# Optimization experiments

Hardware: AMD Instinct MI355X
Metric: run time of the kernel (lower is better)

The kernel has to match this reference:

```python
import jax, jax.numpy as jnp
import numpy as np

D_MODEL = 1024
MEM_HEADS = 4
MEM_KNN = 32
KEY_DIM = 288
VALUE_DIM = 512
Q_RANK = 512
MEM_N_KEYS = 512
TOTAL_KEYS = MEM_N_KEYS * MEM_N_KEYS        # 262144
NUM_BUCKETS = int(np.log2(TOTAL_KEYS))      # 18
BUCKET_DIM = KEY_DIM // NUM_BUCKETS         # 16
BATCH, SEQ = 4, 512


def setup_inputs() -> dict:
    key = jax.random.key(0)
    ks = jax.random.split(key, 7)
    bound = 1.0 / np.sqrt(BUCKET_DIM)
    return {
        "x": jax.random.normal(ks[0], (BATCH, SEQ, D_MODEL), dtype=jnp.float32),
        "keys": jax.random.uniform(ks[1], (MEM_HEADS, NUM_BUCKETS, 2, BUCKET_DIM),
                                   minval=-bound, maxval=bound, dtype=jnp.float32),
        "qd_w": jax.random.normal(ks[2], (Q_RANK, D_MODEL), dtype=jnp.float32) * (1.0 / np.sqrt(D_MODEL)),
        "qd_b": jnp.zeros((Q_RANK,), dtype=jnp.float32),
        "qu_w": jax.random.normal(ks[3], (MEM_HEADS * KEY_DIM, Q_RANK), dtype=jnp.float32) * (1.0 / np.sqrt(Q_RANK)),
        "values": jax.random.normal(ks[4], (TOTAL_KEYS, VALUE_DIM), dtype=jnp.float32) * (VALUE_DIM ** -0.5),
        "vp_w": jax.random.normal(ks[5], (D_MODEL, VALUE_DIM), dtype=jnp.float32) * (1.0 / np.sqrt(VALUE_DIM)),
    }


def _get_indices(query, keys, knn):
    # query: [rows_tok, H, key_dim] flattened per head below. Here query comes
    # in as [N*H, key_dim] reshaped to [N, H, M, bucket_dim].
    N = query.shape[0]
    q = query.reshape(N, MEM_HEADS, NUM_BUCKETS, BUCKET_DIM)
    local = jnp.einsum("nhmd,hmcd->nhmc", q, keys)          # [N,H,M,2]
    s0, s1 = local[..., 0], local[..., 1]
    best_bits = s1 > s0                                      # [N,H,M]
    best_scores = jnp.maximum(s0, s1).sum(-1)                # [N,H]
    deltas = jnp.abs(s0 - s1)                                # [N,H,M]
    bit_weights = (1 << jnp.arange(NUM_BUCKETS, dtype=jnp.int32))
    best_codes = (best_bits.astype(jnp.int32) * bit_weights).sum(-1)  # [N,H]

    rows = N * MEM_HEADS
    deltas = deltas.reshape(rows, NUM_BUCKETS)
    best_scores = best_scores.reshape(rows, 1)
    best_codes = best_codes.reshape(rows, 1)
    knn_eff = min(knn, 1 << NUM_BUCKETS)

    penalties = jnp.zeros((rows, 1), dtype=jnp.float32)
    masks = jnp.zeros((rows, 1), dtype=jnp.int32)
    # Trellis search: unrolled Python loop over a small fixed bucket count (18);
    # candidate width grows 2,4,... then saturates at 2*knn -> static shapes.
    for t in range(NUM_BUCKETS):
        cand_pen = jnp.concatenate([penalties, penalties + deltas[:, t:t + 1]], axis=1)
        cand_msk = jnp.concatenate([masks, masks ^ bit_weights[t]], axis=1)
        step_k = min(knn_eff, cand_pen.shape[1])
        neg_pen, keep = jax.lax.top_k(-cand_pen, step_k)     # smallest penalties, sorted asc
        penalties = -neg_pen
        masks = jnp.take_along_axis(cand_msk, keep, axis=1)
    return best_scores - penalties, best_codes ^ masks        # [rows,knn], [rows,knn]


def reference(x, keys, qd_w, qd_b, qu_w, values, vp_w):
    B, S, D = x.shape
    N = B * S
    x_flat = x.reshape(N, D)
    q = (x_flat @ qd_w.T + qd_b) @ qu_w.T                    # [N, H*key_dim]
    scores, indices = _get_indices(q.reshape(N, MEM_HEADS, KEY_DIM), keys, MEM_KNN)
    scores = jax.nn.softmax(scores, axis=-1)                 # [N*H, knn]
    indices = indices.reshape(N, MEM_HEADS * MEM_KNN)
    scores = scores.reshape(N, MEM_HEADS * MEM_KNN)
    gathered = values[indices]                               # [N, H*knn, value_dim]
    y = jnp.einsum("nk,nkd->nd", scores, gathered)           # embedding_bag mode='sum'
    y = y @ vp_w.T                                           # value_proj (value_dim != d_model)
    return y.reshape(B, S, D_MODEL)
```

## Files before the change

### kernel.cpp

```cpp
#include <hip/hip_runtime.h>
#include <math.h>

#define D_MODEL 1024
#define MEM_HEADS 4
#define KNN 32
#define KEY_DIM 288
#define VALUE_DIM 512
#define Q_RANK 512
#define NUM_BUCKETS 18
#define BUCKET_DIM 16
#define NTOK 2048
#define ROWS (NTOK * MEM_HEADS)
#define QDIM (MEM_HEADS * KEY_DIM)

__global__ __launch_bounds__(256) void gemm_nt_kernel(
    const float* __restrict__ A, const float* __restrict__ B,
    const float* __restrict__ bias, float* __restrict__ C,
    int M, int N, int K)
{
    __shared__ __align__(16) float As[16][68];
    __shared__ __align__(16) float Bs[16][68];

    const int tid  = threadIdx.x;
    const int bm   = blockIdx.y * 64;
    const int bn   = blockIdx.x * 64;
    const int lrow = tid >> 2;
    const int lk   = (tid & 3) * 4;
    const int ty   = tid >> 4;
    const int tx   = tid & 15;

    const float* Aptr = A + (size_t)(bm + lrow) * K + lk;
    const float* Bptr = B + (size_t)(bn + lrow) * K + lk;

    float acc[4][4];
#pragma unroll
    for (int i = 0; i < 4; ++i)
#pragma unroll
        for (int j = 0; j < 4; ++j) acc[i][j] = 0.f;

    for (int k0 = 0; k0 < K; k0 += 16) {
        const float4 a4 = *(const float4*)(Aptr + k0);
        const float4 b4 = *(const float4*)(Bptr + k0);
        __syncthreads();
        As[lk + 0][lrow] = a4.x; As[lk + 1][lrow] = a4.y;
        As[lk + 2][lrow] = a4.z; As[lk + 3][lrow] = a4.w;
        Bs[lk + 0][lrow] = b4.x; Bs[lk + 1][lrow] = b4.y;
        Bs[lk + 2][lrow] = b4.z; Bs[lk + 3][lrow] = b4.w;
        __syncthreads();
#pragma unroll
        for (int kk = 0; kk < 16; ++kk) {
            const float4 af = *(const float4*)&As[kk][ty * 4];
            const float4 bf = *(const float4*)&Bs[kk][tx * 4];
            const float a[4] = {af.x, af.y, af.z, af.w};
            const float b[4] = {bf.x, bf.y, bf.z, bf.w};
#pragma unroll
            for (int i = 0; i < 4; ++i)
#pragma unroll
                for (int j = 0; j < 4; ++j)
                    acc[i][j] += a[i] * b[j];
        }
    }

    float4 bb = {0.f, 0.f, 0.f, 0.f};
    if (bias) bb = *(const float4*)(bias + bn + tx * 4);
#pragma unroll
    for (int i = 0; i < 4; ++i) {
        float4 o;
        o.x = acc[i][0] + bb.x; o.y = acc[i][1] + bb.y;
        o.z = acc[i][2] + bb.z; o.w = acc[i][3] + bb.w;
        *(float4*)(C + (size_t)(bm + ty * 4 + i) * N + bn + tx * 4) = o;
    }
}

__global__ __launch_bounds__(64) void trellis_kernel(
    const float* __restrict__ q, const float* __restrict__ keys,
    float* __restrict__ sc_out, int* __restrict__ idx_out)
{
    __shared__ float s_keys[MEM_HEADS * NUM_BUCKETS * 2 * BUCKET_DIM];
    __shared__ float penB[2][KNN][64];
    __shared__ int   mskB[2][KNN][64];
    __shared__ float dlt[NUM_BUCKETS][64];

    const int tid = threadIdx.x;
    for (int i = tid; i < MEM_HEADS * NUM_BUCKETS * 2 * BUCKET_DIM; i += 64)
        s_keys[i] = keys[i];
    __syncthreads();

    const int r = blockIdx.x * 64 + tid;
    const int h = r & 3;
    const float* qr = q + (size_t)r * KEY_DIM;

    int code = 0;
    for (int m = 0; m < NUM_BUCKETS; ++m) {
        const float* km = s_keys + h * (NUM_BUCKETS * 32) + m * 32;
        float s0 = 0.f, s1 = 0.f;
#pragma unroll
        for (int d = 0; d < BUCKET_DIM; ++d) {
            const float qv = qr[m * BUCKET_DIM + d];
            s0 += qv * km[d];
            s1 += qv * km[16 + d];
        }
        dlt[m][tid] = fabsf(s0 - s1);
        if (s1 > s0) code |= (1 << m);
    }

    penB[0][0][tid] = 0.f;
    mskB[0][0][tid] = 0;
    int nb = 1, cur = 0;
    for (int t = 0; t < NUM_BUCKETS; ++t) {
        const float d = dlt[t][tid];
        const int nk = min(KNN, nb * 2);
        const int nxt = cur ^ 1;
        int i = 0, j = 0;
        for (int o = 0; o < nk; ++o) {
            const float pa = (i < nb) ? penB[cur][i][tid] : 3.4e38f;
            const float pb = (j < nb) ? (penB[cur][j][tid] + d) : 3.4e38f;
            if (pa <= pb) {
                penB[nxt][o][tid] = pa;
                mskB[nxt][o][tid] = mskB[cur][i][tid];
                ++i;
            } else {
                penB[nxt][o][tid] = pb;
                mskB[nxt][o][tid] = mskB[cur][j][tid] ^ (1 << t);
                ++j;
            }
        }
        nb = nk;
        cur = nxt;
    }

    float e[KNN];
    float Z = 0.f;
#pragma unroll
    for (int i = 0; i < KNN; ++i) {
        e[i] = expf(-penB[cur][i][tid]);
        Z += e[i];
    }
    const float inv = 1.0f / Z;
#pragma unroll
    for (int i = 0; i < KNN; ++i) {
        sc_out[(size_t)r * KNN + i]  = e[i] * inv;
        idx_out[(size_t)r * KNN + i] = code ^ mskB[cur][i][tid];
    }
}

__global__ __launch_bounds__(128) void gather_kernel(
    const float* __restrict__ sc, const int* __restrict__ idx,
    const float* __restrict__ values, float* __restrict__ y)
{
    __shared__ float s_s[MEM_HEADS * KNN];
    __shared__ int   s_i[MEM_HEADS * KNN];
    const int n = blockIdx.x;
    const int t = threadIdx.x;
    s_s[t] = sc[(size_t)n * 128 + t];
    s_i[t] = idx[(size_t)n * 128 + t];
    __syncthreads();

    float4 acc = {0.f, 0.f, 0.f, 0.f};
#pragma unroll 4
    for (int k = 0; k < 128; ++k) {
        const float4 v = *(const float4*)(values + (size_t)s_i[k] * VALUE_DIM + t * 4);
        const float w = s_s[k];
        acc.x += w * v.x; acc.y += w * v.y;
        acc.z += w * v.z; acc.w += w * v.w;
    }
    *(float4*)(y + (size_t)n * VALUE_DIM + t * 4) = acc;
}

extern "C" void kernel_launch(void* const* d_in, const int* in_sizes, int n_in,
                              void* d_out, int out_size, void* d_ws, size_t ws_size,
                              hipStream_t stream)
{
    (void)in_sizes; (void)n_in; (void)out_size; (void)ws_size;
    const float* x      = (const float*)d_in[0];
    const float* keys   = (const float*)d_in[1];
    const float* qd_w   = (const float*)d_in[2];
    const float* qd_b   = (const float*)d_in[3];
    const float* qu_w   = (const float*)d_in[4];
    const float* values = (const float*)d_in[5];
    const float* vp_w   = (const float*)d_in[6];
    float* out = (float*)d_out;

    float* q_mid = (float*)d_ws;
    float* q     = q_mid + (size_t)NTOK * Q_RANK;
    float* sc    = q + (size_t)NTOK * QDIM;
    int*   idx   = (int*)(sc + (size_t)ROWS * KNN);
    float* y     = (float*)(idx + (size_t)ROWS * KNN);

    gemm_nt_kernel<<<dim3(Q_RANK / 64, NTOK / 64), 256, 0, stream>>>(
        x, qd_w, qd_b, q_mid, NTOK, Q_RANK, D_MODEL);
    gemm_nt_kernel<<<dim3(QDIM / 64, NTOK / 64), 256, 0, stream>>>(
        q_mid, qu_w, nullptr, q, NTOK, QDIM, Q_RANK);
    trellis_kernel<<<ROWS / 64, 64, 0, stream>>>(q, keys, sc, idx);
    gather_kernel<<<NTOK, 128, 0, stream>>>(sc, idx, values, y);
    gemm_nt_kernel<<<dim3(D_MODEL / 64, NTOK / 64), 256, 0, stream>>>(
        y, vp_w, nullptr, out, NTOK, D_MODEL, VALUE_DIM);
}
```

Before: 902.9 us.

## Use split-bf16 MFMA GEMMs and register-resident deltas in trellis

Replaces the scalar fp32 SIMT GEMM with an MFMA bf16 kernel. It splits each fp32 operand into two or three bf16 pieces and sums the cross products to recover near-fp32 accuracy: three terms for the query projections, which feed discrete top-k selection, and two for the output projection. The trellis kernel now keeps its per-bucket deltas in registers, loads query chunks as float4 and fully unrolls its loops. The gather loop unroll factor goes from 4 to 8. The split precision risks small numeric differences that could flip trellis choices, and the unrolled trellis may raise register pressure.

```diff
diff --git a/kernel.cpp b/kernel.cpp
--- a/kernel.cpp
+++ b/kernel.cpp
@@ -13,62 +13,119 @@
 #define ROWS (NTOK * MEM_HEADS)
 #define QDIM (MEM_HEADS * KEY_DIM)
 
-__global__ __launch_bounds__(256) void gemm_nt_kernel(
+typedef __attribute__((ext_vector_type(8))) short bfrag;
+typedef __attribute__((ext_vector_type(4))) float f32x4;
+
+__device__ __forceinline__ unsigned short f2bf(float x) {
+    unsigned int u = __builtin_bit_cast(unsigned int, x);
+    u += 0x7FFFu + ((u >> 16) & 1u);
+    return (unsigned short)(u >> 16);
+}
+__device__ __forceinline__ float bf2f(unsigned short h) {
+    unsigned int u = ((unsigned int)h) << 16;
+    return __builtin_bit_cast(float, u);
+}
+
+#define LSTR 40
+template<int MODE>
+__global__ __launch_bounds__(256) void gemm_nt_split(
     const float* __restrict__ A, const float* __restrict__ B,
     const float* __restrict__ bias, float* __restrict__ C,
     int M, int N, int K)
 {
-    __shared__ __align__(16) float As[16][68];
-    __shared__ __align__(16) float Bs[16][68];
+    __shared__ __align__(16) unsigned short As[MODE][64][LSTR];
+    __shared__ __align__(16) unsigned short Bs[MODE][64][LSTR];
 
     const int tid  = threadIdx.x;
     const int bm   = blockIdx.y * 64;
     const int bn   = blockIdx.x * 64;
-    const int lrow = tid >> 2;
-    const int lk   = (tid & 3) * 4;
-    const int ty   = tid >> 4;
-    const int tx   = tid & 15;
-
-    const float* Aptr = A + (size_t)(bm + lrow) * K + lk;
-    const float* Bptr = B + (size_t)(bn + lrow) * K + lk;
-
-    float acc[4][4];
-#pragma unroll
-    for (int i = 0; i < 4; ++i)
-#pragma unroll
-        for (int j = 0; j < 4; ++j) acc[i][j] = 0.f;
-
-    for (int k0 = 0; k0 < K; k0 += 16) {
-        const float4 a4 = *(const float4*)(Aptr + k0);
-        const float4 b4 = *(const float4*)(Bptr + k0);
+    const int wave = tid >> 6;
+    const int lane = tid & 63;
+    const int wr   = wave & 1;
+    const int wc   = wave >> 1;
+    const int l15  = lane & 15;
+    const int quad = lane >> 4;
+
+    const int sr = tid >> 2;
+    const int sg = tid & 3;
+
+    f32x4 acc[2][2];
+#pragma unroll
+    for (int i = 0; i < 2; ++i)
+#pragma unroll
+        for (int j = 0; j < 2; ++j) acc[i][j] = (f32x4){0.f, 0.f, 0.f, 0.f};
+
+    const float* Ap = A + (size_t)(bm + sr) * K + sg * 8;
+    const float* Bp = B + (size_t)(bn + sr) * K + sg * 8;
+
+    for (int k0 = 0; k0 < K; k0 += 32) {
+        const float4 a0 = *(const float4*)(Ap + k0);
+        const float4 a1 = *(const float4*)(Ap + k0 + 4);
+        const float4 b0 = *(const float4*)(Bp + k0);
+        const float4 b1 = *(const float4*)(Bp + k0 + 4);
+
         __syncthreads();
-        As[lk + 0][lrow] = a4.x; As[lk + 1][lrow] = a4.y;
-        As[lk + 2][lrow] = a4.z; As[lk + 3][lrow] = a4.w;
-        Bs[lk + 0][lrow] = b4.x; Bs[lk + 1][lrow] = b4.y;
-        Bs[lk + 2][lrow] = b4.z; Bs[lk + 3][lrow] = b4.w;
+        {
+            const float va[8] = {a0.x,a0.y,a0.z,a0.w, a1.x,a1.y,a1.z,a1.w};
+            const float vb[8] = {b0.x,b0.y,b0.z,b0.w, b1.x,b1.y,b1.z,b1.w};
+            bfrag ha[MODE], hb[MODE];
+#pragma unroll
+            for (int i = 0; i < 8; ++i) {
+                float xa = va[i], xb = vb[i];
+#pragma unroll
+                for (int s = 0; s < MODE; ++s) {
+                    const unsigned short sa = f2bf(xa), sb = f2bf(xb);
+                    ha[s][i] = (short)sa; hb[s][i] = (short)sb;
+                    xa -= bf2f(sa);       xb -= bf2f(sb);
+                }
+            }
+#pragma unroll
+            for (int s = 0; s < MODE; ++s) {
+                *(bfrag*)&As[s][sr][sg * 8] = ha[s];
+                *(bfrag*)&Bs[s][sr][sg * 8] = hb[s];
+            }
+        }
         __syncthreads();
-#pragma unroll
-        for (int kk = 0; kk < 16; ++kk) {
-            const float4 af = *(const float4*)&As[kk][ty * 4];
-            const float4 bf = *(const float4*)&Bs[kk][tx * 4];
-            const float a[4] = {af.x, af.y, af.z, af.w};
-            const float b[4] = {bf.x, bf.y, bf.z, bf.w};
-#pragma unroll
-            for (int i = 0; i < 4; ++i)
-#pragma unroll
-                for (int j = 0; j < 4; ++j)
-                    acc[i][j] += a[i] * b[j];
-        }
-    }
-
-    float4 bb = {0.f, 0.f, 0.f, 0.f};
-    if (bias) bb = *(const float4*)(bias + bn + tx * 4);
-#pragma unroll
-    for (int i = 0; i < 4; ++i) {
-        float4 o;
-        o.x = acc[i][0] + bb.x; o.y = acc[i][1] + bb.y;
-        o.z = acc[i][2] + bb.z; o.w = acc[i][3] + bb.w;
-        *(float4*)(C + (size_t)(bm + ty * 4 + i) * N + bn + tx * 4) = o;
+
+        bfrag af[MODE][2], bf[MODE][2];
+#pragma unroll
+        for (int t = 0; t < 2; ++t) {
+            const int mr = wr * 32 + t * 16 + l15;
+            const int nr = wc * 32 + t * 16 + l15;
+#pragma unroll
+            for (int s = 0; s < MODE; ++s) {
+                af[s][t] = *(const bfrag*)&As[s][mr][quad * 8];
+                bf[s][t] = *(const bfrag*)&Bs[s][nr][quad * 8];
+            }
+        }
+#pragma unroll
+        for (int mt = 0; mt < 2; ++mt)
+#pragma unroll
+            for (int nt = 0; nt < 2; ++nt) {
+                f32x4 c = acc[mt][nt];
+                c = __builtin_amdgcn_mfma_f32_16x16x32_bf16(af[0][mt], bf[0][nt], c, 0, 0, 0);
+                c = __builtin_amdgcn_mfma_f32_16x16x32_bf16(af[0][mt], bf[1][nt], c, 0, 0, 0);
+                c = __builtin_amdgcn_mfma_f32_16x16x32_bf16(af[1][mt], bf[0][nt], c, 0, 0, 0);
+                if (MODE == 3) {
+                    c = __builtin_amdgcn_mfma_f32_16x16x32_bf16(af[1][mt], bf[1][nt], c, 0, 0, 0);
+                    c = __builtin_amdgcn_mfma_f32_16x16x32_bf16(af[0][mt], bf[2][nt], c, 0, 0, 0);
+                    c = __builtin_amdgcn_mfma_f32_16x16x32_bf16(af[2][mt], bf[0][nt], c, 0, 0, 0);
+                }
+                acc[mt][nt] = c;
+            }
+    }
+
+#pragma unroll
+    for (int nt = 0; nt < 2; ++nt) {
+        const int col = bn + wc * 32 + nt * 16 + l15;
+        const float bv = bias ? bias[col] : 0.f;
+#pragma unroll
+        for (int mt = 0; mt < 2; ++mt) {
+            const int rowb = bm + wr * 32 + mt * 16 + quad * 4;
+#pragma unroll
+            for (int g = 0; g < 4; ++g)
+                C[(size_t)(rowb + g) * N + col] = acc[mt][nt][g] + bv;
+        }
     }
 }
 
@@ -79,7 +136,6 @@
     __shared__ float s_keys[MEM_HEADS * NUM_BUCKETS * 2 * BUCKET_DIM];
     __shared__ float penB[2][KNN][64];
     __shared__ int   mskB[2][KNN][64];
-    __shared__ float dlt[NUM_BUCKETS][64];
 
     const int tid = threadIdx.x;
     for (int i = tid; i < MEM_HEADS * NUM_BUCKETS * 2 * BUCKET_DIM; i += 64)
@@ -90,25 +146,33 @@
     const int h = r & 3;
     const float* qr = q + (size_t)r * KEY_DIM;
 
+    float dlt[NUM_BUCKETS];
     int code = 0;
+#pragma unroll
     for (int m = 0; m < NUM_BUCKETS; ++m) {
         const float* km = s_keys + h * (NUM_BUCKETS * 32) + m * 32;
+        const float4 q0 = *(const float4*)(qr + m * BUCKET_DIM);
+        const float4 q1 = *(const float4*)(qr + m * BUCKET_DIM + 4);
+        const float4 q2 = *(const float4*)(qr + m * BUCKET_DIM + 8);
+        const float4 q3 = *(const float4*)(qr + m * BUCKET_DIM + 12);
+        const float qv[16] = {q0.x,q0.y,q0.z,q0.w, q1.x,q1.y,q1.z,q1.w,
+                              q2.x,q2.y,q2.z,q2.w, q3.x,q3.y,q3.z,q3.w};
         float s0 = 0.f, s1 = 0.f;
 #pragma unroll
         for (int d = 0; d < BUCKET_DIM; ++d) {
-            const float qv = qr[m * BUCKET_DIM + d];
-            s0 += qv * km[d];
-            s1 += qv * km[16 + d];
-        }
-        dlt[m][tid] = fabsf(s0 - s1);
+            s0 += qv[d] * km[d];
+            s1 += qv[d] * km[16 + d];
+        }
+        dlt[m] = fabsf(s0 - s1);
         if (s1 > s0) code |= (1 << m);
     }
 
     penB[0][0][tid] = 0.f;
     mskB[0][0][tid] = 0;
     int nb = 1, cur = 0;
+#pragma unroll
     for (int t = 0; t < NUM_BUCKETS; ++t) {
-        const float d = dlt[t][tid];
+        const float d = dlt[t];
         const int nk = min(KNN, nb * 2);
         const int nxt = cur ^ 1;
         int i = 0, j = 0;
@@ -157,7 +221,7 @@
     __syncthreads();
 
     float4 acc = {0.f, 0.f, 0.f, 0.f};
-#pragma unroll 4
+#pragma unroll 8
     for (int k = 0; k < 128; ++k) {
         const float4 v = *(const float4*)(values + (size_t)s_i[k] * VALUE_DIM + t * 4);
         const float w = s_s[k];
@@ -187,12 +251,12 @@
     int*   idx   = (int*)(sc + (size_t)ROWS * KNN);
     float* y     = (float*)(idx + (size_t)ROWS * KNN);
 
-    gemm_nt_kernel<<<dim3(Q_RANK / 64, NTOK / 64), 256, 0, stream>>>(
+    gemm_nt_split<3><<<dim3(Q_RANK / 64, NTOK / 64), 256, 0, stream>>>(
         x, qd_w, qd_b, q_mid, NTOK, Q_RANK, D_MODEL);
-    gemm_nt_kernel<<<dim3(QDIM / 64, NTOK / 64), 256, 0, stream>>>(
+    gemm_nt_split<3><<<dim3(QDIM / 64, NTOK / 64), 256, 0, stream>>>(
         q_mid, qu_w, nullptr, q, NTOK, QDIM, Q_RANK);
     trellis_kernel<<<ROWS / 64, 64, 0, stream>>>(q, keys, sc, idx);
     gather_kernel<<<NTOK, 128, 0, stream>>>(sc, idx, values, y);
-    gemm_nt_kernel<<<dim3(D_MODEL / 64, NTOK / 64), 256, 0, stream>>>(
+    gemm_nt_split<2><<<dim3(D_MODEL / 64, NTOK / 64), 256, 0, stream>>>(
         y, vp_w, nullptr, out, NTOK, D_MODEL, VALUE_DIM);
 }
```

New measurement: 871.3 us. 1.04x faster.
